# Optimization experiments

Hardware: AMD Instinct MI355X
Metric: run time of the kernel (lower is better)

The kernel has to match this reference:

```python
import jax, jax.numpy as jnp
import numpy as np

H = 768       # hidden size
NH = 12       # num attention heads
DH = H // NH  # head dim = 64
B = 32
S = 512


def setup_inputs() -> dict:
    key = jax.random.key(0)
    ks = jax.random.split(key, 7)
    scale = 1.0 / np.sqrt(H)
    return {
        "inputs": jax.random.normal(ks[0], (B, S, H), dtype=jnp.float32),
        "Wq": jax.random.normal(ks[1], (H, H), dtype=jnp.float32) * scale,
        "bq": jnp.zeros((H,), dtype=jnp.float32),
        "Wk": jax.random.normal(ks[2], (H, H), dtype=jnp.float32) * scale,
        "bk": jnp.zeros((H,), dtype=jnp.float32),
        "Wv": jax.random.normal(ks[3], (H, H), dtype=jnp.float32) * scale,
        "bv": jnp.zeros((H,), dtype=jnp.float32),
    }


def reference(inputs, Wq, bq, Wk, bk, Wv, bv):
    # BertSelfAttention: linear projections (torch Linear: x @ W.T + b)
    def split_heads(x):  # [B,S,H] -> [B,NH,S,DH]
        return x.reshape(B, S, NH, DH).transpose(0, 2, 1, 3)

    q = split_heads(inputs @ Wq.T + bq)
    k = split_heads(inputs @ Wk.T + bk)
    v = split_heads(inputs @ Wv.T + bv)

    # scores [B,NH,S,S]; the wrapper adds an all-zero attention mask (no-op)
    scores = jnp.einsum("bhqd,bhkd->bhqk", q, k) / jnp.sqrt(jnp.float32(DH))
    probs = jax.nn.softmax(scores, axis=-1)
    ctx = jnp.einsum("bhqk,bhkd->bhqd", probs, v)  # [B,NH,S,DH]
    ctx = ctx.transpose(0, 2, 1, 3).reshape(B, S, H)
    return jnp.tanh(ctx)
```

## Files before the change

kernel.cpp:

```cpp
#include <hip/hip_runtime.h>
#include <hip/hip_bf16.h>
#include <cmath>

#define Bc   32
#define Sc_  512
#define Hc   768
#define NHc  12
#define DHc  64
#define Mc   (Bc * Sc_)
#define Ntot (3 * Hc)

#define QSCALE 0.18033688011112042f

typedef __attribute__((ext_vector_type(8))) short short8v;
typedef __attribute__((ext_vector_type(8))) unsigned short ushort8v;
typedef __attribute__((ext_vector_type(4))) float f32x4;

static __device__ __forceinline__ ushort f2b(float f) {
    __hip_bfloat16 h = __float2bfloat16(f);
    return *reinterpret_cast<ushort*>(&h);
}
static __device__ __forceinline__ ushort2 f2b2(float a, float b) {
    __hip_bfloat162 h = __float22bfloat162_rn(float2{a, b});
    return *reinterpret_cast<ushort2*>(&h);
}

static __device__ __forceinline__ void gl2lds(const ushort* g, ushort* l) {
    __builtin_amdgcn_global_load_lds(
        (const __attribute__((address_space(1))) unsigned int*)g,
        (__attribute__((address_space(3))) unsigned int*)l, 16, 0, 0);
}

static __device__ __forceinline__ float fast_tanh(float x) {
    float e = __builtin_amdgcn_exp2f(x * 2.885390081777927f);
    return 1.0f - 2.0f * __builtin_amdgcn_rcpf(e + 1.0f);
}

__global__ __launch_bounds__(256) void convert_pack(
    const float* __restrict__ X,
    const float* __restrict__ Wq, const float* __restrict__ Wk,
    const float* __restrict__ Wv,
    const float* __restrict__ bq, const float* __restrict__ bk,
    const float* __restrict__ bv,
    ushort* __restrict__ Xt, ushort* __restrict__ Wt, float* __restrict__ bbp)
{
    const int bx = blockIdx.x;
    const int panel = bx / 12, kcg = bx % 12;
    const int t = threadIdx.x;

    __shared__ ushort T[128][68];

    const float* base;
    ushort* out;
    if (panel < 128) {
        base = X + (size_t)panel * 128 * Hc;
        out  = Xt + (size_t)panel * (96 * 1024);
    } else {
        int nblk = panel - 128;
        int n0 = nblk * 128;
        int z = n0 / Hc;
        int nn0 = n0 - z * Hc;
        const float* W = (z == 0) ? Wq : (z == 1) ? Wk : Wv;
        base = W + (size_t)nn0 * Hc;
        out  = Wt + (size_t)nblk * (96 * 1024);
    }
    const int k0 = kcg * 64;

    const int slot = t & 15, rsub = t >> 4;
    #pragma unroll
    for (int rnd = 0; rnd < 8; ++rnd) {
        int row = rnd * 16 + rsub;
        const float* p = base + (size_t)row * Hc + k0 + slot * 4;
        float4 f = *(const float4*)p;
        ushort2 h0 = f2b2(f.x, f.y);
        ushort2 h1 = f2b2(f.z, f.w);
        ushort4 u;
        u.x = h0.x; u.y = h0.y; u.z = h1.x; u.w = h1.y;
        *(ushort4*)&T[row][slot * 4] = u;
    }
    __syncthreads();

    const int row_w = t & 127, kh = t >> 7;
    #pragma unroll
    for (int rnd = 0; rnd < 4; ++rnd) {
        int kc_l = rnd * 2 + kh;
        ushort4 lo = *(const ushort4*)&T[row_w][kc_l * 8];
        ushort4 hi = *(const ushort4*)&T[row_w][kc_l * 8 + 4];
        ushort8v o;
        o[0] = lo.x; o[1] = lo.y; o[2] = lo.z; o[3] = lo.w;
        o[4] = hi.x; o[5] = hi.y; o[6] = hi.z; o[7] = hi.w;
        *(ushort8v*)&out[(size_t)(kcg * 8 + kc_l) * 1024 + row_w * 8] = o;
    }

    if (bx == 0) {
        for (int i = t; i < Ntot; i += 256) {
            int z2 = i / Hc, nn = i - z2 * Hc;
            bbp[i] = ((z2 == 0) ? bq : (z2 == 1) ? bk : bv)[nn];
        }
    }
}

__global__ __launch_bounds__(256) void qkv_mfma(
    const ushort* __restrict__ Xt, const ushort* __restrict__ Wt,
    const float* __restrict__ bbp,
    ushort* __restrict__ Qb, ushort* __restrict__ Kt, ushort* __restrict__ Vt)
{
    const int tid = threadIdx.x;
    const int wave = tid >> 6, lane = tid & 63;
    const int quad = lane >> 4, l16 = lane & 15;
    const int wr = wave >> 1, wc = wave & 1;
    const int m0 = blockIdx.x * 128;
    const int n0 = blockIdx.y * 128;

    __shared__ __align__(16) ushort As[4096];
    __shared__ __align__(16) ushort Bs[4096];

    f32x4 acc[4][4];
    #pragma unroll
    for (int i = 0; i < 4; ++i)
        #pragma unroll
        for (int j = 0; j < 4; ++j) acc[i][j] = (f32x4)(0.f);

    const ushort* gA = Xt + (size_t)blockIdx.x * (96 * 1024) + wave * 1024 + lane * 8;
    const ushort* gB = Wt + (size_t)blockIdx.y * (96 * 1024) + wave * 1024 + lane * 8;
    ushort* lA = As + wave * 1024;
    ushort* lB = Bs + wave * 1024;

    for (int t = 0; t < 24; ++t) {
        const ushort* ga = gA + t * 4096;
        const ushort* gb = gB + t * 4096;
        gl2lds(ga,       lA);
        gl2lds(ga + 512, lA + 512);
        gl2lds(gb,       lB);
        gl2lds(gb + 512, lB + 512);
        __syncthreads();

        short8v a[4], b[4];
        #pragma unroll
        for (int i = 0; i < 4; ++i)
            a[i] = *(const short8v*)&As[quad * 1024 + (wr * 64 + i * 16 + l16) * 8];
        #pragma unroll
        for (int j = 0; j < 4; ++j)
            b[j] = *(const short8v*)&Bs[quad * 1024 + (wc * 64 + j * 16 + l16) * 8];
        #pragma unroll
        for (int i = 0; i < 4; ++i)
            #pragma unroll
            for (int j = 0; j < 4; ++j)
                acc[i][j] = __builtin_amdgcn_mfma_f32_16x16x32_bf16(
                    a[i], b[j], acc[i][j], 0, 0, 0);
        __syncthreads();
    }

    const int z = n0 / Hc;
    #pragma unroll
    for (int j = 0; j < 4; ++j) {
        const int n  = n0 + wc * 64 + j * 16 + l16;
        const int nn = n - z * Hc;
        const int h  = nn >> 6, d = nn & 63;
        const float bias = bbp[n];
        #pragma unroll
        for (int i = 0; i < 4; ++i) {
            const int mbase = m0 + wr * 64 + i * 16 + quad * 4;
            const int bb = mbase >> 9;
            const int s0 = mbase & 511;
            const size_t head = (size_t)(bb * NHc + h) * (Sc_ * DHc);
            if (z == 0) {
                size_t base = head + (size_t)s0 * DHc + d;
                #pragma unroll
                for (int r = 0; r < 4; ++r)
                    Qb[base + (size_t)r * DHc] = f2b((acc[i][j][r] + bias) * QSCALE);
            } else if (z == 1) {
                size_t base = head + (s0 >> 6) * 4096 + (d >> 3) * 512
                            + (s0 & 63) * 8 + (d & 7);
                #pragma unroll
                for (int r = 0; r < 4; ++r)
                    Kt[base + r * 8] = f2b(acc[i][j][r] + bias);
            } else {
                size_t base = head + (s0 >> 6) * 4096 + ((s0 & 63) >> 3) * 512
                            + d * 8 + (s0 & 7);
                ushort4 o;
                o.x = f2b(acc[i][j][0] + bias);
                o.y = f2b(acc[i][j][1] + bias);
                o.z = f2b(acc[i][j][2] + bias);
                o.w = f2b(acc[i][j][3] + bias);
                *(ushort4*)&Vt[base] = o;
            }
        }
    }
}

__global__ __launch_bounds__(256, 2) void attn_mfma(
    const ushort* __restrict__ Qb, const ushort* __restrict__ Kt,
    const ushort* __restrict__ Vt, float* __restrict__ out)
{
    const int bid = blockIdx.x;
    const int super = bid >> 4, l = bid & 15;
    const int head_lin = super * 8 + (l & 7);
    const int qhalf = l >> 3;
    const int b = head_lin / NHc, h = head_lin % NHc;

    const int wave = threadIdx.x >> 6;
    const int lane = threadIdx.x & 63;
    const int quad = lane >> 4, l16 = lane & 15;
    const int q0 = qhalf * 256 + wave * 64;
    const int sw = l16 & 7;

    const size_t head = (size_t)head_lin * (Sc_ * DHc);
    const ushort* __restrict__ Q = Qb + head;
    const ushort* __restrict__ K = Kt + head;
    const ushort* __restrict__ V = Vt + head;

    __shared__ __align__(16) ushort Plds[4][1024];

    short8v aq[4][2];
    #pragma unroll
    for (int u = 0; u < 4; ++u)
        #pragma unroll
        for (int hf = 0; hf < 2; ++hf)
            aq[u][hf] = *(const short8v*)
                &Q[(size_t)(q0 + u * 16 + l16) * DHc + hf * 32 + quad * 8];

    short8v ones;
    #pragma unroll
    for (int i = 0; i < 8; ++i) ones[i] = (short)0x3F80;

    f32x4 o[4][4], rsum[4];
    #pragma unroll
    for (int u = 0; u < 4; ++u) {
        rsum[u] = (f32x4)(0.f);
        #pragma unroll
        for (int t = 0; t < 4; ++t) o[u][t] = (f32x4)(0.f);
    }

    for (int kb = 0; kb < 8; ++kb) {
        const ushort* Kb_ = K + kb * 4096;
        const ushort* Vb_ = V + kb * 4096;

        short8v kf[4][2], vf[4][2];
        #pragma unroll
        for (int t = 0; t < 4; ++t) {
            kf[t][0] = *(const short8v*)&Kb_[quad * 512 + (t * 16 + l16) * 8];
            kf[t][1] = *(const short8v*)&Kb_[(4 + quad) * 512 + (t * 16 + l16) * 8];
            vf[t][0] = *(const short8v*)&Vb_[quad * 512 + (t * 16 + l16) * 8];
            vf[t][1] = *(const short8v*)&Vb_[(4 + quad) * 512 + (t * 16 + l16) * 8];
        }

        #pragma unroll
        for (int u = 0; u < 4; ++u) {
            f32x4 sa[4];
            #pragma unroll
            for (int t = 0; t < 4; ++t) {
                f32x4 s = __builtin_amdgcn_mfma_f32_16x16x32_bf16(
                    kf[t][0], aq[u][0], (f32x4)(0.f), 0, 0, 0);
                sa[t] = __builtin_amdgcn_mfma_f32_16x16x32_bf16(
                    kf[t][1], aq[u][1], s, 0, 0, 0);
            }

            #pragma unroll
            for (int t = 0; t < 4; ++t) {
                float p0 = __builtin_amdgcn_exp2f(sa[t][0]);
                float p1 = __builtin_amdgcn_exp2f(sa[t][1]);
                float p2 = __builtin_amdgcn_exp2f(sa[t][2]);
                float p3 = __builtin_amdgcn_exp2f(sa[t][3]);
                ushort2 lo = f2b2(p0, p1);
                ushort2 hi = f2b2(p2, p3);
                ushort4 pk;
                pk.x = lo.x; pk.y = lo.y; pk.z = hi.x; pk.w = hi.y;
                int c = t * 2 + (quad >> 1);
                int addr = l16 * 64 + ((c ^ sw) * 8) + (quad & 1) * 4;
                *(ushort4*)&Plds[wave][addr] = pk;
            }

            short8v pa0 = *(const short8v*)&Plds[wave][l16 * 64 + ((quad ^ sw) * 8)];
            short8v pa1 = *(const short8v*)&Plds[wave][l16 * 64 + (((4 + quad) ^ sw) * 8)];

            rsum[u] = __builtin_amdgcn_mfma_f32_16x16x32_bf16(
                pa0, ones, rsum[u], 0, 0, 0);
            rsum[u] = __builtin_amdgcn_mfma_f32_16x16x32_bf16(
                pa1, ones, rsum[u], 0, 0, 0);

            #pragma unroll
            for (int t2 = 0; t2 < 4; ++t2) {
                o[u][t2] = __builtin_amdgcn_mfma_f32_16x16x32_bf16(
                    pa0, vf[t2][0], o[u][t2], 0, 0, 0);
                o[u][t2] = __builtin_amdgcn_mfma_f32_16x16x32_bf16(
                    pa1, vf[t2][1], o[u][t2], 0, 0, 0);
            }
        }
    }

    #pragma unroll
    for (int u = 0; u < 4; ++u) {
        #pragma unroll
        for (int r = 0; r < 4; ++r) {
            float inv = __builtin_amdgcn_rcpf(rsum[u][r]);
            int q = q0 + u * 16 + quad * 4 + r;
            size_t base = ((size_t)b * Sc_ + q) * Hc + h * DHc;
            #pragma unroll
            for (int t2 = 0; t2 < 4; ++t2)
                out[base + t2 * 16 + l16] = fast_tanh(o[u][t2][r] * inv);
        }
    }
}

extern "C" void kernel_launch(void* const* d_in, const int* in_sizes, int n_in,
                              void* d_out, int out_size, void* d_ws, size_t ws_size,
                              hipStream_t stream) {
    const float* X  = (const float*)d_in[0];
    const float* Wq = (const float*)d_in[1];
    const float* bq = (const float*)d_in[2];
    const float* Wk = (const float*)d_in[3];
    const float* bk = (const float*)d_in[4];
    const float* Wv = (const float*)d_in[5];
    const float* bv = (const float*)d_in[6];
    float* out = (float*)d_out;

    ushort* Qb  = (ushort*)d_ws;
    ushort* Kt  = Qb + (size_t)Mc * Hc;
    ushort* Vt  = Kt + (size_t)Mc * Hc;
    ushort* Xt  = Vt + (size_t)Mc * Hc;
    ushort* Wt  = Xt + (size_t)Mc * Hc;
    float*  bbp = (float*)(Wt + (size_t)Ntot * Hc);

    convert_pack<<<dim3(1752), 256, 0, stream>>>(
        X, Wq, Wk, Wv, bq, bk, bv, Xt, Wt, bbp);

    dim3 g1(Mc / 128, Ntot / 128);
    qkv_mfma<<<g1, 256, 0, stream>>>(Xt, Wt, bbp, Qb, Kt, Vt);

    attn_mfma<<<dim3(768), 256, 0, stream>>>(Qb, Kt, Vt, out);
}
```

Measured before the change: 219.4 us.

## Rewrite QKV GEMM with 256x256 tiles, double-buffered swizzled LDS and phased pipeline

```diff
diff --git a/kernel.cpp b/kernel.cpp
--- a/kernel.cpp
+++ b/kernel.cpp
@@ -11,6 +11,8 @@
 #define Ntot (3 * Hc)
 
 #define QSCALE 0.18033688011112042f
+
+#define PANEL 196608
 
 typedef __attribute__((ext_vector_type(8))) short short8v;
 typedef __attribute__((ext_vector_type(8))) unsigned short ushort8v;
@@ -52,17 +54,20 @@
 
     const float* base;
     ushort* out;
-    if (panel < 128) {
+    const bool isX = panel < 128;
+    int nhalf = 0;
+    if (isX) {
         base = X + (size_t)panel * 128 * Hc;
-        out  = Xt + (size_t)panel * (96 * 1024);
+        out  = Xt + (size_t)(panel >> 1) * PANEL + (size_t)(panel & 1) * 8192;
     } else {
         int nblk = panel - 128;
+        nhalf = nblk & 1;
         int n0 = nblk * 128;
         int z = n0 / Hc;
         int nn0 = n0 - z * Hc;
         const float* W = (z == 0) ? Wq : (z == 1) ? Wk : Wv;
         base = W + (size_t)nn0 * Hc;
-        out  = Wt + (size_t)nblk * (96 * 1024);
+        out  = Wt + (size_t)(nblk >> 1) * PANEL;
     }
     const int k0 = kcg * 64;
 
@@ -80,16 +85,25 @@
     }
     __syncthreads();
 
-    const int row_w = t & 127, kh = t >> 7;
+    const int row_w = t & 127, khh = t >> 7;
     #pragma unroll
     for (int rnd = 0; rnd < 4; ++rnd) {
-        int kc_l = rnd * 2 + kh;
+        int kc_l = rnd * 2 + khh;
         ushort4 lo = *(const ushort4*)&T[row_w][kc_l * 8];
         ushort4 hi = *(const ushort4*)&T[row_w][kc_l * 8 + 4];
         ushort8v o;
         o[0] = lo.x; o[1] = lo.y; o[2] = lo.z; o[3] = lo.w;
         o[4] = hi.x; o[5] = hi.y; o[6] = hi.z; o[7] = hi.w;
-        *(ushort8v*)&out[(size_t)(kcg * 8 + kc_l) * 1024 + row_w * 8] = o;
+        size_t oidx;
+        if (isX) {
+            oidx = (size_t)kcg * 16384 + (size_t)row_w * 64
+                 + (size_t)((kc_l ^ (row_w & 7)) << 3);
+        } else {
+            int n = nhalf * 128 + row_w;
+            oidx = (size_t)kcg * 16384 + (size_t)(kc_l >> 2) * 8192
+                 + (size_t)n * 32 + (size_t)((((kc_l & 3) ^ ((n >> 1) & 3)) << 3));
+        }
+        *(ushort8v*)&out[oidx] = o;
     }
 
     if (bx == 0) {
@@ -100,90 +114,174 @@
     }
 }
 
-__global__ __launch_bounds__(256) void qkv_mfma(
+static __device__ __forceinline__ void stage_slot(const ushort* g, ushort* l,
+                                                  int wv, int lane) {
+    const int c0 = wv * 1024;
+    gl2lds(g + c0 + lane * 8,       l + c0);
+    gl2lds(g + c0 + 512 + lane * 8, l + c0 + 512);
+}
+
+#define BAR    __builtin_amdgcn_s_barrier()
+#define VMW(n) asm volatile("s_waitcnt vmcnt(" #n ")" ::: "memory")
+
+#define PH_A_READS(kh) \
+    _Pragma("unroll") \
+    for (int mf = 0; mf < 8; ++mf) \
+        a[mf] = *(const short8v*)&As[ab + mf * 1024 + ((((kh) * 4 + quad) ^ rs) << 3)];
+
+#define PH_B_READS(kh, nq) \
+    b0 = *(const short8v*)&Bs[bb + (kh) * 8192 + ((nq) * 2) * 512 + bswz]; \
+    b1 = *(const short8v*)&Bs[bb + (kh) * 8192 + ((nq) * 2 + 1) * 512 + bswz];
+
+#define PH_MFMA(nq) \
+    __builtin_amdgcn_s_setprio(1); \
+    _Pragma("unroll") \
+    for (int mf = 0; mf < 8; ++mf) { \
+        acc[mf][(nq) * 2]     = __builtin_amdgcn_mfma_f32_16x16x32_bf16( \
+            a[mf], b0, acc[mf][(nq) * 2], 0, 0, 0); \
+        acc[mf][(nq) * 2 + 1] = __builtin_amdgcn_mfma_f32_16x16x32_bf16( \
+            a[mf], b1, acc[mf][(nq) * 2 + 1], 0, 0, 0); \
+    } \
+    __builtin_amdgcn_s_setprio(0);
+
+__global__ __launch_bounds__(512, 2) void qkv_mfma(
     const ushort* __restrict__ Xt, const ushort* __restrict__ Wt,
     const float* __restrict__ bbp,
     ushort* __restrict__ Qb, ushort* __restrict__ Kt, ushort* __restrict__ Vt)
 {
+    __shared__ __align__(16) ushort As[32768];
+    __shared__ __align__(16) ushort Bs[32768];
+
     const int tid = threadIdx.x;
-    const int wave = tid >> 6, lane = tid & 63;
+    const int wv = tid >> 6, lane = tid & 63;
     const int quad = lane >> 4, l16 = lane & 15;
-    const int wr = wave >> 1, wc = wave & 1;
-    const int m0 = blockIdx.x * 128;
-    const int n0 = blockIdx.y * 128;
-
-    __shared__ __align__(16) ushort As[4096];
-    __shared__ __align__(16) ushort Bs[4096];
-
-    f32x4 acc[4][4];
-    #pragma unroll
-    for (int i = 0; i < 4; ++i)
+    const int wr = wv >> 2, wc = wv & 3;
+
+    const int bid = blockIdx.x;
+    const int swz = (bid & 7) * 72 + (bid >> 3);
+    const int bx = swz / 9, by = swz % 9;
+
+    const ushort* gA = Xt + (size_t)bx * PANEL;
+    const ushort* gB = Wt + (size_t)by * PANEL;
+
+    f32x4 acc[8][4];
+    #pragma unroll
+    for (int i = 0; i < 8; ++i)
         #pragma unroll
         for (int j = 0; j < 4; ++j) acc[i][j] = (f32x4)(0.f);
 
-    const ushort* gA = Xt + (size_t)blockIdx.x * (96 * 1024) + wave * 1024 + lane * 8;
-    const ushort* gB = Wt + (size_t)blockIdx.y * (96 * 1024) + wave * 1024 + lane * 8;
-    ushort* lA = As + wave * 1024;
-    ushort* lB = Bs + wave * 1024;
-
-    for (int t = 0; t < 24; ++t) {
-        const ushort* ga = gA + t * 4096;
-        const ushort* gb = gB + t * 4096;
-        gl2lds(ga,       lA);
-        gl2lds(ga + 512, lA + 512);
-        gl2lds(gb,       lB);
-        gl2lds(gb + 512, lB + 512);
-        __syncthreads();
-
-        short8v a[4], b[4];
-        #pragma unroll
-        for (int i = 0; i < 4; ++i)
-            a[i] = *(const short8v*)&As[quad * 1024 + (wr * 64 + i * 16 + l16) * 8];
-        #pragma unroll
-        for (int j = 0; j < 4; ++j)
-            b[j] = *(const short8v*)&Bs[quad * 1024 + (wc * 64 + j * 16 + l16) * 8];
-        #pragma unroll
-        for (int i = 0; i < 4; ++i)
-            #pragma unroll
-            for (int j = 0; j < 4; ++j)
-                acc[i][j] = __builtin_amdgcn_mfma_f32_16x16x32_bf16(
-                    a[i], b[j], acc[i][j], 0, 0, 0);
-        __syncthreads();
-    }
-
-    const int z = n0 / Hc;
-    #pragma unroll
-    for (int j = 0; j < 4; ++j) {
-        const int n  = n0 + wc * 64 + j * 16 + l16;
+    const int rs   = l16 & 7;
+    const int bswz = (quad ^ ((l16 >> 1) & 3)) << 3;
+    const int arow = l16 * 64;
+    const int brow = (wc * 64 + l16) * 32;
+
+    short8v a[8], b0, b1;
+
+    stage_slot(gA,        As,        wv, lane);
+    stage_slot(gA + 8192, As + 8192, wv, lane);
+    stage_slot(gB,        Bs,        wv, lane);
+    stage_slot(gB + 8192, Bs + 8192, wv, lane);
+    VMW(2);
+    BAR;
+
+    for (int kt = 0; kt < 11; ++kt) {
+        const int cur = kt & 1;
+        const ushort* gAn = gA + (size_t)(kt + 1) * 16384;
+        const ushort* gBn = gB + (size_t)(kt + 1) * 16384;
+        ushort* lAn = As + (cur ^ 1) * 16384;
+        ushort* lBn = Bs + (cur ^ 1) * 16384;
+        const int ab = cur * 16384 + wr * 8192 + arow;
+        const int bb = cur * 16384 + brow;
+
+        PH_A_READS(0)
+        PH_B_READS(0, 0)
+        stage_slot(gAn, lAn, wv, lane);
+        BAR;
+        PH_MFMA(0)
+        BAR;
+
+        PH_B_READS(0, 1)
+        stage_slot(gAn + 8192, lAn + 8192, wv, lane);
+        BAR;
+        PH_MFMA(1)
+        VMW(4);
+        BAR;
+
+        PH_A_READS(1)
+        PH_B_READS(1, 0)
+        stage_slot(gBn, lBn, wv, lane);
+        BAR;
+        PH_MFMA(0)
+        BAR;
+
+        PH_B_READS(1, 1)
+        stage_slot(gBn + 8192, lBn + 8192, wv, lane);
+        BAR;
+        PH_MFMA(1)
+        VMW(2);
+        BAR;
+    }
+
+    {
+        const int ab = 16384 + wr * 8192 + arow;
+        const int bb = 16384 + brow;
+
+        PH_A_READS(0)
+        PH_B_READS(0, 0)
+        BAR;
+        PH_MFMA(0)
+        BAR;
+
+        PH_B_READS(0, 1)
+        BAR;
+        PH_MFMA(1)
+        VMW(0);
+        BAR;
+
+        PH_A_READS(1)
+        PH_B_READS(1, 0)
+        BAR;
+        PH_MFMA(0)
+        BAR;
+
+        PH_B_READS(1, 1)
+        BAR;
+        PH_MFMA(1)
+    }
+
+    const int z = by / 3;
+    #pragma unroll
+    for (int nf = 0; nf < 4; ++nf) {
+        const int n  = by * 256 + wc * 64 + nf * 16 + l16;
         const int nn = n - z * Hc;
         const int h  = nn >> 6, d = nn & 63;
         const float bias = bbp[n];
         #pragma unroll
-        for (int i = 0; i < 4; ++i) {
-            const int mbase = m0 + wr * 64 + i * 16 + quad * 4;
-            const int bb = mbase >> 9;
+        for (int mf = 0; mf < 8; ++mf) {
+            const int mbase = bx * 256 + wr * 128 + mf * 16 + quad * 4;
+            const int bb2 = mbase >> 9;
             const int s0 = mbase & 511;
-            const size_t head = (size_t)(bb * NHc + h) * (Sc_ * DHc);
+            const size_t head = (size_t)(bb2 * NHc + h) * (Sc_ * DHc);
             if (z == 0) {
-                size_t base = head + (size_t)s0 * DHc + d;
+                size_t basep = head + (size_t)s0 * DHc + d;
                 #pragma unroll
                 for (int r = 0; r < 4; ++r)
-                    Qb[base + (size_t)r * DHc] = f2b((acc[i][j][r] + bias) * QSCALE);
+                    Qb[basep + (size_t)r * DHc] = f2b((acc[mf][nf][r] + bias) * QSCALE);
             } else if (z == 1) {
-                size_t base = head + (s0 >> 6) * 4096 + (d >> 3) * 512
-                            + (s0 & 63) * 8 + (d & 7);
+                size_t basep = head + (s0 >> 6) * 4096 + (d >> 3) * 512
+                             + (s0 & 63) * 8 + (d & 7);
                 #pragma unroll
                 for (int r = 0; r < 4; ++r)
-                    Kt[base + r * 8] = f2b(acc[i][j][r] + bias);
+                    Kt[basep + r * 8] = f2b(acc[mf][nf][r] + bias);
             } else {
-                size_t base = head + (s0 >> 6) * 4096 + ((s0 & 63) >> 3) * 512
-                            + d * 8 + (s0 & 7);
+                size_t basep = head + (s0 >> 6) * 4096 + ((s0 & 63) >> 3) * 512
+                             + d * 8 + (s0 & 7);
                 ushort4 o;
-                o.x = f2b(acc[i][j][0] + bias);
-                o.y = f2b(acc[i][j][1] + bias);
-                o.z = f2b(acc[i][j][2] + bias);
-                o.w = f2b(acc[i][j][3] + bias);
-                *(ushort4*)&Vt[base] = o;
+                o.x = f2b(acc[mf][nf][0] + bias);
+                o.y = f2b(acc[mf][nf][1] + bias);
+                o.z = f2b(acc[mf][nf][2] + bias);
+                o.w = f2b(acc[mf][nf][3] + bias);
+                *(ushort4*)&Vt[basep] = o;
             }
         }
     }
@@ -325,8 +423,7 @@
     convert_pack<<<dim3(1752), 256, 0, stream>>>(
         X, Wq, Wk, Wv, bq, bk, bv, Xt, Wt, bbp);
 
-    dim3 g1(Mc / 128, Ntot / 128);
-    qkv_mfma<<<g1, 256, 0, stream>>>(Xt, Wt, bbp, Qb, Kt, Vt);
+    qkv_mfma<<<dim3(576), 512, 0, stream>>>(Xt, Wt, bbp, Qb, Kt, Vt);
 
     attn_mfma<<<dim3(768), 256, 0, stream>>>(Qb, Kt, Vt, out);
 }
```

After: 241.4 us. 10.0% more time.

## Fuse QKV projection into attention kernel with LDS-resident K and V

Applied to the files above, without the earlier changes.

```diff
diff --git a/kernel.cpp b/kernel.cpp
--- a/kernel.cpp
+++ b/kernel.cpp
@@ -23,12 +23,6 @@
 static __device__ __forceinline__ ushort2 f2b2(float a, float b) {
     __hip_bfloat162 h = __float22bfloat162_rn(float2{a, b});
     return *reinterpret_cast<ushort2*>(&h);
-}
-
-static __device__ __forceinline__ void gl2lds(const ushort* g, ushort* l) {
-    __builtin_amdgcn_global_load_lds(
-        (const __attribute__((address_space(1))) unsigned int*)g,
-        (__attribute__((address_space(3))) unsigned int*)l, 16, 0, 0);
 }
 
 static __device__ __forceinline__ float fast_tanh(float x) {
@@ -100,141 +94,158 @@
     }
 }
 
-__global__ __launch_bounds__(256) void qkv_mfma(
+__global__ __launch_bounds__(512, 2) void fused_qkv_attn(
     const ushort* __restrict__ Xt, const ushort* __restrict__ Wt,
-    const float* __restrict__ bbp,
-    ushort* __restrict__ Qb, ushort* __restrict__ Kt, ushort* __restrict__ Vt)
-{
-    const int tid = threadIdx.x;
-    const int wave = tid >> 6, lane = tid & 63;
-    const int quad = lane >> 4, l16 = lane & 15;
-    const int wr = wave >> 1, wc = wave & 1;
-    const int m0 = blockIdx.x * 128;
-    const int n0 = blockIdx.y * 128;
-
-    __shared__ __align__(16) ushort As[4096];
-    __shared__ __align__(16) ushort Bs[4096];
-
-    f32x4 acc[4][4];
-    #pragma unroll
-    for (int i = 0; i < 4; ++i)
-        #pragma unroll
-        for (int j = 0; j < 4; ++j) acc[i][j] = (f32x4)(0.f);
-
-    const ushort* gA = Xt + (size_t)blockIdx.x * (96 * 1024) + wave * 1024 + lane * 8;
-    const ushort* gB = Wt + (size_t)blockIdx.y * (96 * 1024) + wave * 1024 + lane * 8;
-    ushort* lA = As + wave * 1024;
-    ushort* lB = Bs + wave * 1024;
-
-    for (int t = 0; t < 24; ++t) {
-        const ushort* ga = gA + t * 4096;
-        const ushort* gb = gB + t * 4096;
-        gl2lds(ga,       lA);
-        gl2lds(ga + 512, lA + 512);
-        gl2lds(gb,       lB);
-        gl2lds(gb + 512, lB + 512);
-        __syncthreads();
-
-        short8v a[4], b[4];
-        #pragma unroll
-        for (int i = 0; i < 4; ++i)
-            a[i] = *(const short8v*)&As[quad * 1024 + (wr * 64 + i * 16 + l16) * 8];
-        #pragma unroll
-        for (int j = 0; j < 4; ++j)
-            b[j] = *(const short8v*)&Bs[quad * 1024 + (wc * 64 + j * 16 + l16) * 8];
-        #pragma unroll
-        for (int i = 0; i < 4; ++i)
-            #pragma unroll
-            for (int j = 0; j < 4; ++j)
-                acc[i][j] = __builtin_amdgcn_mfma_f32_16x16x32_bf16(
-                    a[i], b[j], acc[i][j], 0, 0, 0);
-        __syncthreads();
-    }
-
-    const int z = n0 / Hc;
-    #pragma unroll
-    for (int j = 0; j < 4; ++j) {
-        const int n  = n0 + wc * 64 + j * 16 + l16;
-        const int nn = n - z * Hc;
-        const int h  = nn >> 6, d = nn & 63;
-        const float bias = bbp[n];
-        #pragma unroll
-        for (int i = 0; i < 4; ++i) {
-            const int mbase = m0 + wr * 64 + i * 16 + quad * 4;
-            const int bb = mbase >> 9;
-            const int s0 = mbase & 511;
-            const size_t head = (size_t)(bb * NHc + h) * (Sc_ * DHc);
-            if (z == 0) {
-                size_t base = head + (size_t)s0 * DHc + d;
-                #pragma unroll
-                for (int r = 0; r < 4; ++r)
-                    Qb[base + (size_t)r * DHc] = f2b((acc[i][j][r] + bias) * QSCALE);
-            } else if (z == 1) {
-                size_t base = head + (s0 >> 6) * 4096 + (d >> 3) * 512
-                            + (s0 & 63) * 8 + (d & 7);
-                #pragma unroll
-                for (int r = 0; r < 4; ++r)
-                    Kt[base + r * 8] = f2b(acc[i][j][r] + bias);
-            } else {
-                size_t base = head + (s0 >> 6) * 4096 + ((s0 & 63) >> 3) * 512
-                            + d * 8 + (s0 & 7);
-                ushort4 o;
-                o.x = f2b(acc[i][j][0] + bias);
-                o.y = f2b(acc[i][j][1] + bias);
-                o.z = f2b(acc[i][j][2] + bias);
-                o.w = f2b(acc[i][j][3] + bias);
-                *(ushort4*)&Vt[base] = o;
-            }
-        }
-    }
-}
-
-__global__ __launch_bounds__(256, 2) void attn_mfma(
-    const ushort* __restrict__ Qb, const ushort* __restrict__ Kt,
-    const ushort* __restrict__ Vt, float* __restrict__ out)
+    const float* __restrict__ bbp, float* __restrict__ out)
 {
     const int bid = blockIdx.x;
-    const int super = bid >> 4, l = bid & 15;
-    const int head_lin = super * 8 + (l & 7);
-    const int qhalf = l >> 3;
+    const int head_lin = bid >> 1;
+    const int qhalf = bid & 1;
     const int b = head_lin / NHc, h = head_lin % NHc;
 
-    const int wave = threadIdx.x >> 6;
-    const int lane = threadIdx.x & 63;
+    const int tid = threadIdx.x;
+    const int wv = tid >> 6, lane = tid & 63;
     const int quad = lane >> 4, l16 = lane & 15;
-    const int q0 = qhalf * 256 + wave * 64;
-    const int sw = l16 & 7;
-
-    const size_t head = (size_t)head_lin * (Sc_ * DHc);
-    const ushort* __restrict__ Q = Qb + head;
-    const ushort* __restrict__ K = Kt + head;
-    const ushort* __restrict__ V = Vt + head;
-
-    __shared__ __align__(16) ushort Plds[4][1024];
-
-    short8v aq[4][2];
-    #pragma unroll
-    for (int u = 0; u < 4; ++u)
+
+    __shared__ __align__(16) ushort Klds[32768];
+    __shared__ __align__(16) ushort Vlds[32768];
+    __shared__ __align__(16) ushort Plds[8][1024];
+
+    const int ph  = h >> 1;
+    const int cwb = (h & 1) * 64;
+
+    f32x4 qacc[2][4];
+    #pragma unroll
+    for (int i = 0; i < 2; ++i)
+        #pragma unroll
+        for (int j = 0; j < 4; ++j) qacc[i][j] = (f32x4)(0.f);
+
+    const int sq0 = qhalf * 256 + wv * 32;
+
+    #pragma unroll 2
+    for (int t = 0; t < 24; ++t) {
+        const size_t kgo = (size_t)(t * 4 + quad) * 1024;
+        short8v a[2], bw[4];
+        #pragma unroll
+        for (int i = 0; i < 2; ++i) {
+            int m = b * 512 + sq0 + i * 16 + l16;
+            a[i] = *(const short8v*)&Xt[(size_t)(m >> 7) * (96 * 1024) + kgo
+                                        + (m & 127) * 8];
+        }
+        #pragma unroll
+        for (int j = 0; j < 4; ++j)
+            bw[j] = *(const short8v*)&Wt[(size_t)ph * (96 * 1024) + kgo
+                                         + (cwb + j * 16 + l16) * 8];
+        #pragma unroll
+        for (int i = 0; i < 2; ++i)
+            #pragma unroll
+            for (int j = 0; j < 4; ++j)
+                qacc[i][j] = __builtin_amdgcn_mfma_f32_16x16x32_bf16(
+                    a[i], bw[j], qacc[i][j], 0, 0, 0);
+    }
+
+    ushort* Qscr = Klds;
+    #pragma unroll
+    for (int j = 0; j < 4; ++j) {
+        const float bias = bbp[h * 64 + j * 16 + l16];
+        #pragma unroll
+        for (int i = 0; i < 2; ++i) {
+            const int ql = wv * 32 + i * 16 + quad * 4;
+            #pragma unroll
+            for (int r = 0; r < 4; ++r)
+                Qscr[(ql + r) * 64 + j * 16 + l16] =
+                    f2b((qacc[i][j][r] + bias) * QSCALE);
+        }
+    }
+    __syncthreads();
+
+    short8v aq[2][2];
+    #pragma unroll
+    for (int u = 0; u < 2; ++u)
         #pragma unroll
         for (int hf = 0; hf < 2; ++hf)
             aq[u][hf] = *(const short8v*)
-                &Q[(size_t)(q0 + u * 16 + l16) * DHc + hf * 32 + quad * 8];
+                &Qscr[(wv * 32 + u * 16 + l16) * 64 + hf * 32 + quad * 8];
+    __syncthreads();
+
+    f32x4 kacc[4][4], vacc[4][4];
+    #pragma unroll
+    for (int i = 0; i < 4; ++i)
+        #pragma unroll
+        for (int j = 0; j < 4; ++j) { kacc[i][j] = (f32x4)(0.f); vacc[i][j] = (f32x4)(0.f); }
+
+    const int sk0 = wv * 64;
+
+    #pragma unroll 2
+    for (int t = 0; t < 24; ++t) {
+        const size_t kgo = (size_t)(t * 4 + quad) * 1024;
+        short8v a[4], bk_[4], bv_[4];
+        #pragma unroll
+        for (int i = 0; i < 4; ++i) {
+            int m = b * 512 + sk0 + i * 16 + l16;
+            a[i] = *(const short8v*)&Xt[(size_t)(m >> 7) * (96 * 1024) + kgo
+                                        + (m & 127) * 8];
+        }
+        #pragma unroll
+        for (int j = 0; j < 4; ++j) {
+            bk_[j] = *(const short8v*)&Wt[(size_t)(6 + ph) * (96 * 1024) + kgo
+                                          + (cwb + j * 16 + l16) * 8];
+            bv_[j] = *(const short8v*)&Wt[(size_t)(12 + ph) * (96 * 1024) + kgo
+                                          + (cwb + j * 16 + l16) * 8];
+        }
+        #pragma unroll
+        for (int i = 0; i < 4; ++i)
+            #pragma unroll
+            for (int j = 0; j < 4; ++j) {
+                kacc[i][j] = __builtin_amdgcn_mfma_f32_16x16x32_bf16(
+                    a[i], bk_[j], kacc[i][j], 0, 0, 0);
+                vacc[i][j] = __builtin_amdgcn_mfma_f32_16x16x32_bf16(
+                    a[i], bv_[j], vacc[i][j], 0, 0, 0);
+            }
+    }
+
+    #pragma unroll
+    for (int j = 0; j < 4; ++j) {
+        const int d = j * 16 + l16;
+        const float biask = bbp[768 + h * 64 + d];
+        const float biasv = bbp[1536 + h * 64 + d];
+        #pragma unroll
+        for (int i = 0; i < 4; ++i) {
+            const int s0 = sk0 + i * 16 + quad * 4;
+            const int baseK = (s0 >> 6) * 4096 + (d >> 3) * 512
+                            + (s0 & 63) * 8 + (d & 7);
+            #pragma unroll
+            for (int r = 0; r < 4; ++r)
+                Klds[baseK + r * 8] = f2b(kacc[i][j][r] + biask);
+            const int baseV = (s0 >> 6) * 4096 + ((s0 & 63) >> 3) * 512
+                            + d * 8 + (s0 & 7);
+            ushort4 o4;
+            o4.x = f2b(vacc[i][j][0] + biasv);
+            o4.y = f2b(vacc[i][j][1] + biasv);
+            o4.z = f2b(vacc[i][j][2] + biasv);
+            o4.w = f2b(vacc[i][j][3] + biasv);
+            *(ushort4*)&Vlds[baseV] = o4;
+        }
+    }
+    __syncthreads();
+
+    const int sw = l16 & 7;
 
     short8v ones;
     #pragma unroll
     for (int i = 0; i < 8; ++i) ones[i] = (short)0x3F80;
 
-    f32x4 o[4][4], rsum[4];
-    #pragma unroll
-    for (int u = 0; u < 4; ++u) {
+    f32x4 o[2][4], rsum[2];
+    #pragma unroll
+    for (int u = 0; u < 2; ++u) {
         rsum[u] = (f32x4)(0.f);
         #pragma unroll
         for (int t = 0; t < 4; ++t) o[u][t] = (f32x4)(0.f);
     }
 
     for (int kb = 0; kb < 8; ++kb) {
-        const ushort* Kb_ = K + kb * 4096;
-        const ushort* Vb_ = V + kb * 4096;
+        const ushort* Kb_ = Klds + kb * 4096;
+        const ushort* Vb_ = Vlds + kb * 4096;
 
         short8v kf[4][2], vf[4][2];
         #pragma unroll
@@ -246,7 +257,7 @@
         }
 
         #pragma unroll
-        for (int u = 0; u < 4; ++u) {
+        for (int u = 0; u < 2; ++u) {
             f32x4 sa[4];
             #pragma unroll
             for (int t = 0; t < 4; ++t) {
@@ -268,11 +279,11 @@
                 pk.x = lo.x; pk.y = lo.y; pk.z = hi.x; pk.w = hi.y;
                 int c = t * 2 + (quad >> 1);
                 int addr = l16 * 64 + ((c ^ sw) * 8) + (quad & 1) * 4;
-                *(ushort4*)&Plds[wave][addr] = pk;
+                *(ushort4*)&Plds[wv][addr] = pk;
             }
 
-            short8v pa0 = *(const short8v*)&Plds[wave][l16 * 64 + ((quad ^ sw) * 8)];
-            short8v pa1 = *(const short8v*)&Plds[wave][l16 * 64 + (((4 + quad) ^ sw) * 8)];
+            short8v pa0 = *(const short8v*)&Plds[wv][l16 * 64 + ((quad ^ sw) * 8)];
+            short8v pa1 = *(const short8v*)&Plds[wv][l16 * 64 + (((4 + quad) ^ sw) * 8)];
 
             rsum[u] = __builtin_amdgcn_mfma_f32_16x16x32_bf16(
                 pa0, ones, rsum[u], 0, 0, 0);
@@ -290,11 +301,11 @@
     }
 
     #pragma unroll
-    for (int u = 0; u < 4; ++u) {
+    for (int u = 0; u < 2; ++u) {
         #pragma unroll
         for (int r = 0; r < 4; ++r) {
             float inv = __builtin_amdgcn_rcpf(rsum[u][r]);
-            int q = q0 + u * 16 + quad * 4 + r;
+            int q = qhalf * 256 + wv * 32 + u * 16 + quad * 4 + r;
             size_t base = ((size_t)b * Sc_ + q) * Hc + h * DHc;
             #pragma unroll
             for (int t2 = 0; t2 < 4; ++t2)
@@ -321,12 +332,10 @@
     ushort* Xt  = Vt + (size_t)Mc * Hc;
     ushort* Wt  = Xt + (size_t)Mc * Hc;
     float*  bbp = (float*)(Wt + (size_t)Ntot * Hc);
+    (void)Kt; (void)Vt;
 
     convert_pack<<<dim3(1752), 256, 0, stream>>>(
         X, Wq, Wk, Wv, bq, bk, bv, Xt, Wt, bbp);
 
-    dim3 g1(Mc / 128, Ntot / 128);
-    qkv_mfma<<<g1, 256, 0, stream>>>(Xt, Wt, bbp, Qb, Kt, Vt);
-
-    attn_mfma<<<dim3(768), 256, 0, stream>>>(Qb, Kt, Vt, out);
-}
+    fused_qkv_attn<<<dim3(768), 512, 0, stream>>>(Xt, Wt, bbp, out);
+}
```

Measured after the change: 237.8 us. 8.4% more time.
